# Kernel optimization log

Hardware: AMD Instinct MI355X
Metric: run time of the kernel (lower is better)

Reference implementation:

```python
import jax, jax.numpy as jnp
import numpy as np

B, S, D = 2, 2048, 1024
H, HD = 16, 64
MAX_OFF = 64
FC_LAYERS = 4


def _rope_tables(seq_len, head_dim):
    inv_freq = 1.0 / (10000.0 ** (jnp.arange(0, head_dim, 2, dtype=jnp.float32) / head_dim))
    t = jnp.arange(seq_len, dtype=jnp.float32)
    freqs = jnp.einsum('s,d->sd', t, inv_freq)
    emb = jnp.concatenate([freqs, freqs], axis=-1)  # [S, HD]
    return jnp.cos(emb), jnp.sin(emb)


def _rotate_half(x):
    h = x.shape[-1] // 2
    return jnp.concatenate([-x[..., h:], x[..., :h]], axis=-1)


def _fc_mask(bar_ids, instrument_ids):
    # rule tables indexed by clamped bar offset (key_bar - query_bar) + MAX_OFF
    same_rules = jnp.zeros(2 * MAX_OFF + 1, dtype=bool).at[MAX_OFF:].set(True)
    cross_rules = (jnp.zeros(2 * MAX_OFF + 1, dtype=bool)
                   .at[MAX_OFF:MAX_OFF + 3].set(True)
                   .at[MAX_OFF + 4].set(True))
    off = jnp.clip(bar_ids[:, None, :] - bar_ids[:, :, None], -MAX_OFF, MAX_OFF) + MAX_OFF  # [B,S,S]
    k_real = instrument_ids[:, None, :] < 129
    q_real = instrument_ids[:, :, None] < 129
    same = (instrument_ids[:, None, :] == instrument_ids[:, :, None]) & k_real & q_real
    diff = (~same) & k_real & q_real
    mask = (same & same_rules[off]) | (diff & cross_rules[off])
    # global key tokens (instrument 129 or bar -1) visible to every query
    is_global_k = (instrument_ids[:, None, :] == 129) | (bar_ids[:, None, :] == -1)  # [B,1,S]
    mask = mask | is_global_k
    s = bar_ids.shape[1]
    causal = jnp.tril(jnp.ones((s, s), dtype=bool))
    return mask & causal[None]  # [B,S,S]


def setup_inputs() -> dict:
    key = jax.random.key(0)
    ks = jax.random.split(key, 12)
    sc = 1.0 / np.sqrt(D)
    return {
        'x': jax.random.normal(ks[0], (B, S, D), jnp.float32),
        'bar_ids': jnp.sort(jax.random.randint(ks[1], (B, S), 0, 128), axis=-1),
        'instrument_ids': jax.random.randint(ks[2], (B, S), 0, 130),
        'layer_idx': 0,
        'Wq': jax.random.normal(ks[3], (D, D), jnp.float32) * sc,
        'bq': jnp.zeros((D,), jnp.float32),
        'Wk': jax.random.normal(ks[4], (D, D), jnp.float32) * sc,
        'bk': jnp.zeros((D,), jnp.float32),
        'Wv': jax.random.normal(ks[5], (D, D), jnp.float32) * sc,
        'bv': jnp.zeros((D,), jnp.float32),
        'Wo': jax.random.normal(ks[6], (D, D), jnp.float32) * sc,
        'bo': jnp.zeros((D,), jnp.float32),
    }


def reference(x, bar_ids, instrument_ids, layer_idx, Wq, bq, Wk, bk, Wv, bv, Wo, bo):
    b, s, d = x.shape
    q = (x @ Wq + bq).reshape(b, s, H, HD).transpose(0, 2, 1, 3)  # [B,H,S,HD]
    k = (x @ Wk + bk).reshape(b, s, H, HD).transpose(0, 2, 1, 3)
    v = (x @ Wv + bv).reshape(b, s, H, HD).transpose(0, 2, 1, 3)
    cos, sin = _rope_tables(s, HD)  # [S,HD], broadcasts over [B,H,S,HD]
    q = q * cos + _rotate_half(q) * sin
    k = k * cos + _rotate_half(k) * sin
    if layer_idx < FC_LAYERS:
        mask = _fc_mask(bar_ids, instrument_ids)  # [B,S,S]
    else:
        mask = jnp.broadcast_to(jnp.tril(jnp.ones((s, s), dtype=bool)), (b, s, s))
    bias = jnp.where(mask[:, None, :, :], 0.0, -jnp.inf).astype(x.dtype)
    scores = jnp.einsum('bhqd,bhkd->bhqk', q, k) * (HD ** -0.5) + bias
    attn = jax.nn.softmax(scores, axis=-1)
    out = jnp.einsum('bhqk,bhkd->bhqd', attn, v)
    out = out.transpose(0, 2, 1, 3).reshape(b, s, d)
    return out @ Wo + bo
```

## Files before the change

### kernel.cpp

```cpp
#include <hip/hip_runtime.h>
#include <hip/hip_bf16.h>

typedef unsigned short u16;
typedef unsigned u32;
typedef unsigned long long u64;
typedef float f32x4 __attribute__((ext_vector_type(4)));
typedef __bf16 bf16x8 __attribute__((ext_vector_type(8)));

#define NB 2
#define NS 2048
#define ND 1024
#define NH 16
#define HD 64

__device__ inline u16 bfbits(float f) { __bf16 h = (__bf16)f; return __builtin_bit_cast(u16, h); }

__device__ inline void gl16(const u16* g, u16* l) {
  __builtin_amdgcn_global_load_lds((const __attribute__((address_space(1))) void*)(g),
                                   (__attribute__((address_space(3))) void*)(l), 16, 0, 0);
}

__global__ void __launch_bounds__(256)
prep_all(const float* __restrict__ W0, const float* __restrict__ W1,
         const float* __restrict__ W2, const float* __restrict__ W3,
         u16* __restrict__ T0, u16* __restrict__ T1, u16* __restrict__ T2, u16* __restrict__ T3,
         const float* __restrict__ x, u16* __restrict__ xb,
         float* __restrict__ cost, float* __restrict__ sint) {
  const int bid = blockIdx.x, t = threadIdx.x;
  if (bid < 4096) {
    __shared__ float tile[32][33];
    const float* Ws[4] = {W0, W1, W2, W3};
    u16* Ts[4] = {T0, T1, T2, T3};
    const float* __restrict__ W = Ws[bid >> 10];
    u16* __restrict__ WT = Ts[bid >> 10];
    const int rem = bid & 1023;
    const int n0 = (rem & 31) * 32, k0 = (rem >> 5) * 32;
    const int tx = t & 31, ty = t >> 5;
#pragma unroll
    for (int i = 0; i < 4; ++i)
      tile[ty + i * 8][tx] = W[(size_t)(k0 + ty + i * 8) * ND + n0 + tx];
    __syncthreads();
#pragma unroll
    for (int i = 0; i < 4; ++i)
      WT[(size_t)(n0 + ty + i * 8) * ND + k0 + tx] = bfbits(tile[tx][ty + i * 8]);
  } else if (bid < 8192) {
    const int i = (bid - 4096) * 256 + t;
    float4 v = reinterpret_cast<const float4*>(x)[i];
    uint2 pk;
    pk.x = (unsigned)bfbits(v.x) | ((unsigned)bfbits(v.y) << 16);
    pk.y = (unsigned)bfbits(v.z) | ((unsigned)bfbits(v.w) << 16);
    reinterpret_cast<uint2*>(xb)[i] = pk;
  } else {
    const int i = (bid - 8192) * 256 + t;
    const int s = i >> 5, d = i & 31;
    float invf = powf(10000.f, -(float)d / 32.f);
    float a = (float)s * invf;
    cost[i] = cosf(a);
    sint[i] = sinf(a);
  }
}

__global__ void __launch_bounds__(512, 2)
gemm_qkv(const u16* __restrict__ A, const u16* __restrict__ BT3,
         const float* __restrict__ bq, const float* __restrict__ bk, const float* __restrict__ bv,
         u16* __restrict__ qbuf, u16* __restrict__ kbuf, u16* __restrict__ vtbuf,
         const float* __restrict__ cost, const float* __restrict__ sint,
         const int* __restrict__ bar, const int* __restrict__ inst,
         const int* __restrict__ lidx, u64* __restrict__ mb, u32* __restrict__ tilebits) {
  constexpr int K = ND;
  __shared__ alignas(16) u16 Alds[2][256][64];
  __shared__ alignas(16) u16 Blds[2][256][64];
  const int t = threadIdx.x;
  const int hid = (int)blockIdx.x;

  if (hid >= 192) {
    int* sbar = reinterpret_cast<int*>(&Alds[0][0][0]);
    int* sinst = sbar + NB * NS;
    int* firsts = reinterpret_cast<int*>(&Blds[0][0][0]);
    int* lasts = firsts + NB * 128;
    u64* Gw = reinterpret_cast<u64*>(lasts + NB * 128);
    for (int i = t; i < NB * NS; i += 512) {
      sbar[i] = bar[i];
      sinst[i] = inst[i];
    }
    __syncthreads();
    for (int i = t; i < NB * NS; i += 512) {
      const int idx = i & (NS - 1);
      const int v = sbar[i];
      if (v >= 0 && v < 128) {
        if (idx == 0 || sbar[i - 1] != v) firsts[(i >> 11) * 128 + v] = idx;
        if (idx == NS - 1 || sbar[i + 1] != v) lasts[(i >> 11) * 128 + v] = idx;
      }
    }
    {
      const int w8 = t >> 6, lane = t & 63;
#pragma unroll
      for (int p8 = 0; p8 < 8; ++p8) {
        const int p = w8 * 8 + p8;
        const int gb = p >> 5, gkt = p & 31;
        const int k = gkt * 64 + lane;
        const bool gbit = (sinst[gb * NS + k] == 129) || (sbar[gb * NS + k] == -1);
        const u64 wd = __ballot(gbit);
        if (lane == 0) Gw[p] = wd;
      }
    }
    __syncthreads();
    const bool fc = (lidx[0] < 4);
    const int w8 = t >> 6, lane = t & 63;
    const int gw = (hid - 192) * 8 + w8;
#pragma unroll
    for (int rr = 0; rr < 8; ++rr) {
      const int pair = gw + 512 * rr;
      const int b = pair >> 11, q = pair & (NS - 1);
      const int qt = q >> 6;
      const int qb = sbar[b * NS + q];
      const bool qreal = sinst[b * NS + q] < 129;
      int lo = NS, hi = -1;
      if (fc && qreal && qb >= 0 && qb < 128) {
        lo = firsts[b * 128 + qb];
        hi = lasts[b * 128 + qb];
      }
      const int kt = lane;
      if (kt <= qt) {
        u64 word;
        if (!fc) {
          word = ~0ULL;
        } else {
          word = Gw[b * 32 + kt];
          const int base = kt * 64;
          const int s = lo - base, e = hi - base;
          if (e >= 0 && s <= 63) {
            const int cs = s < 0 ? 0 : s;
            const int ce = e > 63 ? 63 : e;
            u64 m = (ce >= 63) ? ~0ULL : ((1ULL << (ce + 1)) - 1);
            if (cs > 0) m &= ~((1ULL << cs) - 1);
            word |= m;
          }
        }
        if (kt == qt) {
          const int qq = q & 63;
          word &= (qq >= 63) ? ~0ULL : ((1ULL << (qq + 1)) - 1);
        }
        mb[(((size_t)b * NS + q) << 5) + kt] = word;
      }
    }
    if (hid == 192 && w8 == 0) {
      const int b = lane >> 5, qt = lane & 31;
      u32 tbw;
      if (!fc) {
        tbw = (qt >= 31) ? 0xFFFFFFFFu : ((1u << (qt + 1)) - 1);
      } else {
        const int v0 = sbar[b * NS + qt * 64];
        const int v1 = sbar[b * NS + qt * 64 + 63];
        const int lo_t = (v0 >= 0 && v0 < 128) ? firsts[b * 128 + v0] : 0;
        const int hi_t = (v1 >= 0 && v1 < 128) ? lasts[b * 128 + v1] : NS - 1;
        tbw = 0;
        for (int kt = 0; kt <= qt; ++kt) {
          const bool on = (kt == qt) || (Gw[b * 32 + kt] != 0ULL) ||
                          (kt * 64 <= hi_t && kt * 64 + 63 >= lo_t);
          if (on) tbw |= (1u << kt);
        }
      }
      if (lane < 64) tilebits[lane] = tbw;
    }
    return;
  }

  const int m0 = (hid / 12) << 8;
  const int nblk = hid % 12;
  const int proj = nblk >> 2;
  const int n0 = (nblk & 3) << 8;
  const int w = t >> 6, lane = t & 63, lr = lane & 15, lg = lane >> 4;
  const int wm = w >> 2, wn = w & 3;
  const float* __restrict__ bias = proj == 0 ? bq : (proj == 1 ? bk : bv);
  f32x4 acc[8][4] = {};

  const int srow = lane >> 3;
  const int lcol = (lane & 7) ^ srow;
  const u16* Ag = A + (size_t)(m0 + w * 32 + srow) * K + lcol * 8;
  const u16* Bg = BT3 + (size_t)(proj * ND + n0 + w * 32 + srow) * K + lcol * 8;
  const int swz = lr & 7;

#pragma unroll
  for (int c = 0; c < 4; ++c) {
    gl16(Ag + (size_t)c * 8 * K, &Alds[0][w * 32 + c * 8][0]);
    gl16(Bg + (size_t)c * 8 * K, &Blds[0][w * 32 + c * 8][0]);
  }

  for (int s = 0; s < K / 64; ++s) {
    asm volatile("s_waitcnt vmcnt(0)" ::: "memory");
    __builtin_amdgcn_s_barrier();
    if (s + 1 < K / 64) {
      const int k0n = (s + 1) * 64;
#pragma unroll
      for (int c = 0; c < 4; ++c) {
        gl16(Ag + k0n + (size_t)c * 8 * K, &Alds[(s + 1) & 1][w * 32 + c * 8][0]);
        gl16(Bg + k0n + (size_t)c * 8 * K, &Blds[(s + 1) & 1][w * 32 + c * 8][0]);
      }
    }
    const int cur = s & 1;
    bf16x8 bfr[4][2];
#pragma unroll
    for (int ni = 0; ni < 4; ++ni)
#pragma unroll
      for (int ks = 0; ks < 2; ++ks)
        bfr[ni][ks] = *reinterpret_cast<const bf16x8*>(
            &Blds[cur][wn * 64 + ni * 16 + lr][(((ks << 2) + lg) ^ swz) << 3]);
#pragma unroll
    for (int mi = 0; mi < 8; ++mi) {
#pragma unroll
      for (int ks = 0; ks < 2; ++ks) {
        const bf16x8 af = *reinterpret_cast<const bf16x8*>(
            &Alds[cur][wm * 128 + mi * 16 + lr][(((ks << 2) + lg) ^ swz) << 3]);
#pragma unroll
        for (int ni = 0; ni < 4; ++ni)
          acc[mi][ni] = __builtin_amdgcn_mfma_f32_16x16x32_bf16(af, bfr[ni][ks], acc[mi][ni], 0, 0, 0);
      }
    }
  }

  if (proj < 2) {
    u16* out = proj ? kbuf : qbuf;
    const float qs = proj == 0 ? 0.18033688f : 1.0f;
    const int colbase = n0 + wn * 64;
    const int h = colbase >> 6;
#pragma unroll
    for (int mi = 0; mi < 8; ++mi)
#pragma unroll
      for (int r = 0; r < 4; ++r) {
        const int row = m0 + wm * 128 + mi * 16 + lg * 4 + r;
        const int b = row >> 11, s = row & (NS - 1);
        u16* op = out + ((size_t)(b * NH + h) * NS + s) * HD;
#pragma unroll
        for (int nf = 0; nf < 2; ++nf) {
          const int dlo = nf * 16 + lr;
          float lo = acc[mi][nf][r] + bias[colbase + dlo];
          float hi = acc[mi][nf + 2][r] + bias[colbase + dlo + 32];
          float c = cost[s * 32 + dlo], si = sint[s * 32 + dlo];
          const u32 pk = (u32)bfbits((lo * c - hi * si) * qs) |
                         ((u32)bfbits((hi * c + lo * si) * qs) << 16);
          *reinterpret_cast<u32*>(op + 2 * dlo) = pk;
        }
      }
  } else {
    u16* out = vtbuf;
#pragma unroll
    for (int mi = 0; mi < 8; ++mi)
#pragma unroll
      for (int ni = 0; ni < 4; ++ni) {
        const int col = n0 + wn * 64 + ni * 16 + lr;
        const int h = col >> 6, d = col & 63;
        const int s0 = m0 + wm * 128 + mi * 16 + lg * 4;
        const int b = s0 >> 11, s = s0 & (NS - 1);
        uint2 pk;
        pk.x = (unsigned)bfbits(acc[mi][ni][0] + bias[col]) |
               ((unsigned)bfbits(acc[mi][ni][1] + bias[col]) << 16);
        pk.y = (unsigned)bfbits(acc[mi][ni][2] + bias[col]) |
               ((unsigned)bfbits(acc[mi][ni][3] + bias[col]) << 16);
        *reinterpret_cast<uint2*>(out + ((size_t)(b * NH + h) * HD + d) * NS + s) = pk;
      }
  }
}

__global__ void __launch_bounds__(256)
gemm_out(const u16* __restrict__ A, const u16* __restrict__ BT, const float* __restrict__ bias,
         float* __restrict__ out) {
  constexpr int K = ND;
  __shared__ alignas(16) u16 Alds[3][128][32];
  __shared__ alignas(16) u16 Blds[3][64][32];
  const int t = threadIdx.x;
  const int hid = (int)blockIdx.x + 16 * (int)blockIdx.y;
  const int xcd = hid & 7, j = hid >> 3;
  const int m0 = ((xcd >> 1) * 8 + (j >> 3)) * 128;
  const int n0 = ((xcd & 1) * 8 + (j & 7)) * 64;
  const int w = t >> 6, lane = t & 63, lr = lane & 15, lg = lane >> 4;
  f32x4 acc[2][4] = {};

  const int srow = lane >> 2;
  const int scol = (lane & 3) * 8;
  const u16* Ag = A + (size_t)(m0 + w * 32 + srow) * K + scol;
  const u16* Bg = BT + (size_t)(n0 + w * 16 + srow) * K + scol;

#pragma unroll
  for (int p = 0; p < 2; ++p) {
    gl16(Ag + p * 32, &Alds[p][w * 32][0]);
    gl16(Ag + p * 32 + 16 * K, &Alds[p][w * 32 + 16][0]);
    gl16(Bg + p * 32, &Blds[p][w * 16][0]);
  }

  int cur = 0;
  for (int k0 = 0; k0 < K; k0 += 32) {
    if (k0 + 32 < K) {
      asm volatile("s_waitcnt vmcnt(3)" ::: "memory");
    } else {
      asm volatile("s_waitcnt vmcnt(0)" ::: "memory");
    }
    __builtin_amdgcn_s_barrier();
    if (k0 + 64 < K) {
      int bn = cur + 2;
      if (bn >= 3) bn -= 3;
      gl16(Ag + k0 + 64, &Alds[bn][w * 32][0]);
      gl16(Ag + k0 + 64 + 16 * K, &Alds[bn][w * 32 + 16][0]);
      gl16(Bg + k0 + 64, &Blds[bn][w * 16][0]);
    }
    bf16x8 af[2], bfr[4];
#pragma unroll
    for (int i = 0; i < 2; ++i)
      af[i] = *reinterpret_cast<const bf16x8*>(&Alds[cur][w * 32 + i * 16 + lr][lg * 8]);
#pragma unroll
    for (int i = 0; i < 4; ++i)
      bfr[i] = *reinterpret_cast<const bf16x8*>(&Blds[cur][i * 16 + lr][lg * 8]);
#pragma unroll
    for (int mi = 0; mi < 2; ++mi)
#pragma unroll
      for (int ni = 0; ni < 4; ++ni)
        acc[mi][ni] = __builtin_amdgcn_mfma_f32_16x16x32_bf16(af[mi], bfr[ni], acc[mi][ni], 0, 0, 0);
    cur = (cur == 2) ? 0 : cur + 1;
  }

#pragma unroll
  for (int mi = 0; mi < 2; ++mi)
#pragma unroll
    for (int r = 0; r < 4; ++r) {
      const int row = m0 + w * 32 + mi * 16 + lg * 4 + r;
#pragma unroll
      for (int ni = 0; ni < 4; ++ni) {
        const int col = n0 + ni * 16 + lr;
        out[(size_t)row * ND + col] = acc[mi][ni][r] + bias[col];
      }
    }
}

__global__ void __launch_bounds__(256, 4)
attn_fused(const u16* __restrict__ qb, const u16* __restrict__ kb, const u16* __restrict__ vtb,
           const u64* __restrict__ mb, const u32* __restrict__ tilebits,
           u16* __restrict__ attnout) {
  __shared__ alignas(16) u16 Klds[2][64][64];
  __shared__ alignas(16) u16 Vlds[2][64][64];
  __shared__ alignas(16) u16 Plds[4][16][64];
  const int t = threadIdx.x, w = t >> 6, lane = t & 63, lr = lane & 15, lg = lane >> 4;
  const int hid = (int)blockIdx.x;
  const int xcd = hid & 7, ix = hid >> 3;
  const int g = ix >> 5, r0 = ix & 31;
  const int bh = xcd * 4 + (r0 >> 3);
  const int b = bh >> 4, h = bh & 15;
  const int j = r0 & 7;
  const int qt = (g == 0) ? 31 - j : (g == 1) ? j : (g == 2) ? 23 - j : 8 + j;
  const int qbase = qt * 64;
  const u16* __restrict__ qh = qb + (size_t)(b * NH + h) * NS * HD;
  const u16* __restrict__ kh = kb + (size_t)(b * NH + h) * NS * HD;
  const u16* __restrict__ vth = vtb + (size_t)(b * NH + h) * HD * NS;
  const u32 bits = tilebits[b * 32 + qt];
  const int nt = __popc(bits);

  const int srow = lane >> 3;
  const int lcol = (lane & 7) ^ srow;
  const int sw = lr & 7;

  const int qrow = qbase + w * 16 + lr;
  const bf16x8 qf0 = *reinterpret_cast<const bf16x8*>(qh + (size_t)qrow * HD + lg * 8);
  const bf16x8 qf1 = *reinterpret_cast<const bf16x8*>(qh + (size_t)qrow * HD + 32 + lg * 8);
  const u64* __restrict__ mrow = mb + (((size_t)b * NS + qrow) << 5);

  float m_s = -1e30f, l_s = 0.f;
  f32x4 oacc[4] = {};
  int cur = 0;

  const int kt0 = __ffs(bits) - 1;
  u32 rem = bits & (bits - 1);
  {
    const int kb0 = kt0 << 6;
#pragma unroll
    for (int c = 0; c < 2; ++c) {
      const int row = w * 16 + c * 8 + srow;
      gl16(kh + (size_t)(kb0 + row) * HD + lcol * 8, &Klds[0][w * 16 + c * 8][0]);
      gl16(vth + (size_t)row * NS + kb0 + lcol * 8, &Vlds[0][w * 16 + c * 8][0]);
    }
  }
  u64 mw = mrow[kt0];

  for (int i = 0; i < nt; ++i) {
    __syncthreads();
    u64 mwn = 0ULL;
    if (rem) {
      const int ktn = __ffs(rem) - 1;
      rem &= rem - 1;
      const int kb0n = ktn << 6;
#pragma unroll
      for (int c = 0; c < 2; ++c) {
        const int row = w * 16 + c * 8 + srow;
        gl16(kh + (size_t)(kb0n + row) * HD + lcol * 8, &Klds[cur ^ 1][w * 16 + c * 8][0]);
        gl16(vth + (size_t)row * NS + kb0n + lcol * 8, &Vlds[cur ^ 1][w * 16 + c * 8][0]);
      }
      mwn = mrow[ktn];
    }

    if (!__all(mw == 0ULL)) {
      const u16* Kb = &Klds[cur][0][0];
      const u16* Vb = &Vlds[cur][0][0];

      f32x4 sacc[4] = {};
      __builtin_amdgcn_s_setprio(1);
#pragma unroll
      for (int n = 0; n < 4; ++n) {
        const u16* kr = Kb + (n * 16 + lr) * 64;
        bf16x8 kf0 = *reinterpret_cast<const bf16x8*>(kr + ((lg ^ sw) << 3));
        bf16x8 kf1 = *reinterpret_cast<const bf16x8*>(kr + (((4 + lg) ^ sw) << 3));
        sacc[n] = __builtin_amdgcn_mfma_f32_16x16x32_bf16(kf0, qf0, sacc[n], 0, 0, 0);
        sacc[n] = __builtin_amdgcn_mfma_f32_16x16x32_bf16(kf1, qf1, sacc[n], 0, 0, 0);
      }
      __builtin_amdgcn_s_setprio(0);

      float pm[4][4];
      float mx4[4];
#pragma unroll
      for (int n = 0; n < 4; ++n) {
#pragma unroll
        for (int r = 0; r < 4; ++r) {
          const bool vis = (mw >> (n * 16 + lg * 4 + r)) & 1ULL;
          pm[n][r] = vis ? sacc[n][r] : -3e30f;
        }
        mx4[n] = fmaxf(fmaxf(pm[n][0], pm[n][1]), fmaxf(pm[n][2], pm[n][3]));
      }
      float mx = fmaxf(fmaxf(mx4[0], mx4[1]), fmaxf(mx4[2], mx4[3]));
      mx = fmaxf(mx, __shfl_xor(mx, 16));
      mx = fmaxf(mx, __shfl_xor(mx, 32));

      const bool skip = __all(mx <= m_s + 11.5415603f);
      const float mn = skip ? m_s : fmaxf(m_s, mx);

      float rs = 0.f;
#pragma unroll
      for (int n = 0; n < 4; ++n) {
        const float e0 = exp2f(pm[n][0] - mn);
        const float e1 = exp2f(pm[n][1] - mn);
        const float e2 = exp2f(pm[n][2] - mn);
        const float e3 = exp2f(pm[n][3] - mn);
        rs += (e0 + e1) + (e2 + e3);
        uint2 pk;
        pk.x = (unsigned)bfbits(e0) | ((unsigned)bfbits(e1) << 16);
        pk.y = (unsigned)bfbits(e2) | ((unsigned)bfbits(e3) << 16);
        *reinterpret_cast<uint2*>(&Plds[w][lr][(((n << 2) + lg) ^ (lr & 14)) << 2]) = pk;
      }
      rs += __shfl_xor(rs, 16);
      rs += __shfl_xor(rs, 32);

      if (skip) {
        l_s += rs;
      } else {
        const float sf = exp2f(m_s - mn);
        m_s = mn;
        l_s = l_s * sf + rs;
        float sfr[4];
#pragma unroll
        for (int r = 0; r < 4; ++r) sfr[r] = __shfl(sf, lg * 4 + r);
#pragma unroll
        for (int nd = 0; nd < 4; ++nd)
#pragma unroll
          for (int r = 0; r < 4; ++r) oacc[nd][r] *= sfr[r];
      }

      const bf16x8 pf0 = *reinterpret_cast<const bf16x8*>(&Plds[w][lr][((2 * lg) ^ (lr & 14)) << 2]);
      const bf16x8 pf1 = *reinterpret_cast<const bf16x8*>(&Plds[w][lr][((8 + 2 * lg) ^ (lr & 14)) << 2]);
      __builtin_amdgcn_s_setprio(1);
#pragma unroll
      for (int nd = 0; nd < 4; ++nd) {
        const u16* vr = Vb + (nd * 16 + lr) * 64;
        bf16x8 vf0 = *reinterpret_cast<const bf16x8*>(vr + ((lg ^ sw) << 3));
        bf16x8 vf1 = *reinterpret_cast<const bf16x8*>(vr + (((4 + lg) ^ sw) << 3));
        oacc[nd] = __builtin_amdgcn_mfma_f32_16x16x32_bf16(pf0, vf0, oacc[nd], 0, 0, 0);
        oacc[nd] = __builtin_amdgcn_mfma_f32_16x16x32_bf16(pf1, vf1, oacc[nd], 0, 0, 0);
      }
      __builtin_amdgcn_s_setprio(0);
    }

    mw = mwn;
    cur ^= 1;
  }

  float il[4];
#pragma unroll
  for (int r = 0; r < 4; ++r) il[r] = 1.f / __shfl(l_s, lg * 4 + r);
#pragma unroll
  for (int nd = 0; nd < 4; ++nd)
#pragma unroll
    for (int r = 0; r < 4; ++r) {
      const int i = qbase + w * 16 + lg * 4 + r;
      attnout[(size_t)(b * NS + i) * ND + h * HD + nd * 16 + lr] = bfbits(oacc[nd][r] * il[r]);
    }
}

extern "C" void kernel_launch(void* const* d_in, const int* in_sizes, int n_in,
                              void* d_out, int out_size, void* d_ws, size_t ws_size,
                              hipStream_t stream) {
  const float* x = (const float*)d_in[0];
  const int* bar = (const int*)d_in[1];
  const int* inst = (const int*)d_in[2];
  const int* lidx = (const int*)d_in[3];
  const float* Wq = (const float*)d_in[4];
  const float* bq = (const float*)d_in[5];
  const float* Wk = (const float*)d_in[6];
  const float* bk = (const float*)d_in[7];
  const float* Wv = (const float*)d_in[8];
  const float* bv = (const float*)d_in[9];
  const float* Wo = (const float*)d_in[10];
  const float* bo = (const float*)d_in[11];
  float* out = (float*)d_out;

  char* ws = (char*)d_ws;
  constexpr size_t XB = (size_t)NB * NS * ND * 2;
  constexpr size_t WT = (size_t)ND * ND * 2;
  u16* xb   = (u16*)(ws);
  u16* WqT  = (u16*)(ws + XB);
  u16* WkT  = (u16*)(ws + XB + 1 * WT);
  u16* WvT  = (u16*)(ws + XB + 2 * WT);
  u16* WoT  = (u16*)(ws + XB + 3 * WT);
  u16* qbuf = (u16*)(ws + XB + 4 * WT);
  u16* kbuf = (u16*)(ws + XB + 4 * WT + XB);
  u16* vtbuf= (u16*)(ws + XB + 4 * WT + 2 * XB);
  float* cost = (float*)(ws + XB + 4 * WT + 3 * XB);
  float* sint = cost + NS * 32;
  u64* maskbuf = (u64*)(ws + XB + 4 * WT + 3 * XB + (size_t)NS * 32 * 4 * 2);
  u32* tilebits = (u32*)((char*)maskbuf + (size_t)NB * NS * 32 * 8);
  u16* attnout = xb;

  prep_all<<<dim3(8448), 256, 0, stream>>>(Wq, Wk, Wv, Wo, WqT, WkT, WvT, WoT,
                                           x, xb, cost, sint);

  gemm_qkv<<<dim3(256), 512, 0, stream>>>(xb, WqT, bq, bk, bv, qbuf, kbuf, vtbuf, cost, sint,
                                          bar, inst, lidx, maskbuf, tilebits);

  attn_fused<<<dim3(1024), 256, 0, stream>>>(qbuf, kbuf, vtbuf, maskbuf, tilebits, attnout);

  gemm_out<<<dim3(16, 32), 256, 0, stream>>>(attnout, WoT, bo, out);
}
```

Baseline: 113.1 us.

## Retile output projection GEMM to 128x128 tiles with swizzled LDS and BK=64

Reworks the output projection GEMM from 128x64 tiles with 256 threads and K-step 32 to 128x128 tiles with 512 threads (8 waves in a 4x2 grid) and K-step 64. It adds an XOR swizzle on the LDS column index to avoid bank conflicts, and switches to a simpler 1D grid of 256 blocks without the XCD-aware mapping. The larger tile improves data reuse and halves the number of barriers, at the cost of more LDS per block, fewer blocks, and losing the previous XCD-aware block placement.

Result: faster. 109.8 us (median of 2 runs) (-3.0%).

```diff
diff --git a/kernel.cpp b/kernel.cpp
--- a/kernel.cpp
+++ b/kernel.cpp
@@ -262,59 +262,71 @@
   }
 }
 
-__global__ void __launch_bounds__(256)
+__global__ void __launch_bounds__(512)
 gemm_out(const u16* __restrict__ A, const u16* __restrict__ BT, const float* __restrict__ bias,
          float* __restrict__ out) {
   constexpr int K = ND;
-  __shared__ alignas(16) u16 Alds[3][128][32];
-  __shared__ alignas(16) u16 Blds[3][64][32];
+  __shared__ alignas(16) u16 Alds[3][128][64];
+  __shared__ alignas(16) u16 Blds[3][128][64];
   const int t = threadIdx.x;
-  const int hid = (int)blockIdx.x + 16 * (int)blockIdx.y;
-  const int xcd = hid & 7, j = hid >> 3;
-  const int m0 = ((xcd >> 1) * 8 + (j >> 3)) * 128;
-  const int n0 = ((xcd & 1) * 8 + (j & 7)) * 64;
+  const int hid = (int)blockIdx.x;
+  const int n0 = (hid & 7) * 128;
+  const int m0 = (hid >> 3) * 128;
   const int w = t >> 6, lane = t & 63, lr = lane & 15, lg = lane >> 4;
+  const int wm = w >> 1, wn = w & 1;
   f32x4 acc[2][4] = {};
 
-  const int srow = lane >> 2;
-  const int scol = (lane & 3) * 8;
-  const u16* Ag = A + (size_t)(m0 + w * 32 + srow) * K + scol;
-  const u16* Bg = BT + (size_t)(n0 + w * 16 + srow) * K + scol;
+  const int srow = lane >> 3;
+  const int lcol = (lane & 7) ^ srow;
+  const u16* Ag = A + (size_t)(m0 + w * 16 + srow) * K + lcol * 8;
+  const u16* Bg = BT + (size_t)(n0 + w * 16 + srow) * K + lcol * 8;
+  const int swz = lr & 7;
 
 #pragma unroll
   for (int p = 0; p < 2; ++p) {
-    gl16(Ag + p * 32, &Alds[p][w * 32][0]);
-    gl16(Ag + p * 32 + 16 * K, &Alds[p][w * 32 + 16][0]);
-    gl16(Bg + p * 32, &Blds[p][w * 16][0]);
+#pragma unroll
+    for (int c = 0; c < 2; ++c) {
+      gl16(Ag + p * 64 + (size_t)c * 8 * K, &Alds[p][w * 16 + c * 8][0]);
+      gl16(Bg + p * 64 + (size_t)c * 8 * K, &Blds[p][w * 16 + c * 8][0]);
+    }
   }
 
   int cur = 0;
-  for (int k0 = 0; k0 < K; k0 += 32) {
-    if (k0 + 32 < K) {
-      asm volatile("s_waitcnt vmcnt(3)" ::: "memory");
+  for (int s = 0; s < K / 64; ++s) {
+    if (s + 1 < K / 64) {
+      asm volatile("s_waitcnt vmcnt(4)" ::: "memory");
     } else {
       asm volatile("s_waitcnt vmcnt(0)" ::: "memory");
     }
     __builtin_amdgcn_s_barrier();
-    if (k0 + 64 < K) {
+    if (s + 2 < K / 64) {
       int bn = cur + 2;
       if (bn >= 3) bn -= 3;
-      gl16(Ag + k0 + 64, &Alds[bn][w * 32][0]);
-      gl16(Ag + k0 + 64 + 16 * K, &Alds[bn][w * 32 + 16][0]);
-      gl16(Bg + k0 + 64, &Blds[bn][w * 16][0]);
-    }
-    bf16x8 af[2], bfr[4];
-#pragma unroll
-    for (int i = 0; i < 2; ++i)
-      af[i] = *reinterpret_cast<const bf16x8*>(&Alds[cur][w * 32 + i * 16 + lr][lg * 8]);
-#pragma unroll
-    for (int i = 0; i < 4; ++i)
-      bfr[i] = *reinterpret_cast<const bf16x8*>(&Blds[cur][i * 16 + lr][lg * 8]);
-#pragma unroll
-    for (int mi = 0; mi < 2; ++mi)
-#pragma unroll
-      for (int ni = 0; ni < 4; ++ni)
-        acc[mi][ni] = __builtin_amdgcn_mfma_f32_16x16x32_bf16(af[mi], bfr[ni], acc[mi][ni], 0, 0, 0);
+      const int k0n = (s + 2) * 64;
+#pragma unroll
+      for (int c = 0; c < 2; ++c) {
+        gl16(Ag + k0n + (size_t)c * 8 * K, &Alds[bn][w * 16 + c * 8][0]);
+        gl16(Bg + k0n + (size_t)c * 8 * K, &Blds[bn][w * 16 + c * 8][0]);
+      }
+    }
+    bf16x8 bfr[4][2];
+#pragma unroll
+    for (int ni = 0; ni < 4; ++ni)
+#pragma unroll
+      for (int ks = 0; ks < 2; ++ks)
+        bfr[ni][ks] = *reinterpret_cast<const bf16x8*>(
+            &Blds[cur][wn * 64 + ni * 16 + lr][(((ks << 2) + lg) ^ swz) << 3]);
+#pragma unroll
+    for (int mi = 0; mi < 2; ++mi) {
+#pragma unroll
+      for (int ks = 0; ks < 2; ++ks) {
+        const bf16x8 af = *reinterpret_cast<const bf16x8*>(
+            &Alds[cur][wm * 32 + mi * 16 + lr][(((ks << 2) + lg) ^ swz) << 3]);
+#pragma unroll
+        for (int ni = 0; ni < 4; ++ni)
+          acc[mi][ni] = __builtin_amdgcn_mfma_f32_16x16x32_bf16(af, bfr[ni][ks], acc[mi][ni], 0, 0, 0);
+      }
+    }
     cur = (cur == 2) ? 0 : cur + 1;
   }
 
@@ -322,10 +334,10 @@
   for (int mi = 0; mi < 2; ++mi)
 #pragma unroll
     for (int r = 0; r < 4; ++r) {
-      const int row = m0 + w * 32 + mi * 16 + lg * 4 + r;
+      const int row = m0 + wm * 32 + mi * 16 + lg * 4 + r;
 #pragma unroll
       for (int ni = 0; ni < 4; ++ni) {
-        const int col = n0 + ni * 16 + lr;
+        const int col = n0 + wn * 64 + ni * 16 + lr;
         out[(size_t)row * ND + col] = acc[mi][ni][r] + bias[col];
       }
     }
@@ -532,5 +544,5 @@
 
   attn_fused<<<dim3(1024), 256, 0, stream>>>(qbuf, kbuf, vtbuf, maskbuf, tilebits, attnout);
 
-  gemm_out<<<dim3(16, 32), 256, 0, stream>>>(attnout, WoT, bo, out);
+  gemm_out<<<dim3(256), 512, 0, stream>>>(attnout, WoT, bo, out);
 }
```
